# Optimization experiments

Hardware: AMD Instinct MI355X
Metric: run time of the kernel (lower is better)

The kernel has to match this reference:

```python
import jax, jax.numpy as jnp
import numpy as np

B, N, DIN, DOUT, H = 4, 2048, 512, 512, 8
HD = DOUT // H


def setup_inputs() -> dict:
    key = jax.random.key(0)
    ks = jax.random.split(key, 8)
    x = jax.random.normal(ks[0], (B, N, DIN), dtype=jnp.float32)
    mask = jax.random.randint(ks[1], (B, 1, N, N), 0, 2, dtype=jnp.int32)
    s = 1.0 / np.sqrt(DIN)
    Wq = jax.random.uniform(ks[2], (DOUT, DIN), jnp.float32, -s, s)
    Wk = jax.random.uniform(ks[3], (DOUT, DIN), jnp.float32, -s, s)
    Wv = jax.random.uniform(ks[4], (DOUT, DIN), jnp.float32, -s, s)
    bq = jax.random.uniform(ks[5], (DOUT,), jnp.float32, -s, s)
    bk = jax.random.uniform(ks[6], (DOUT,), jnp.float32, -s, s)
    bv = jax.random.uniform(ks[7], (DOUT,), jnp.float32, -s, s)
    return {"x": x, "Wq": Wq, "bq": bq, "Wk": Wk, "bk": bk, "Wv": Wv, "bv": bv, "mask": mask}


def reference(x, Wq, bq, Wk, bk, Wv, bv, mask):
    b, n, _ = x.shape
    # torch Linear: y = x @ W.T + b ; split heads -> [b, h, n, hd]
    def proj(W, bias):
        y = jnp.einsum('bnd,od->bno', x, W) + bias
        return y.reshape(b, n, H, HD).transpose(0, 2, 1, 3)
    Q, K, V = proj(Wq, bq), proj(Wk, bk), proj(Wv, bv)
    scores = jnp.einsum('bhnd,bhmd->bhnm', Q, K) / np.sqrt(HD).astype(np.float32)
    scores = jnp.where(mask == 0, jnp.float32(-1e9), scores)
    attn = jax.nn.softmax(scores, axis=-1)
    ctx = jnp.einsum('bhnm,bhmd->bhnd', attn, V)
    ctx = ctx.transpose(0, 2, 1, 3).reshape(b, n, DOUT)
    return jax.nn.elu(ctx)
```

## Files before the change

kernel.cpp:

```cpp
#include <hip/hip_runtime.h>
#include <math.h>
#include <stdint.h>

#define CB 4
#define CN 2048
#define CDIN 512
#define CDOUT 512
#define CH 8
#define CHD 64
#define CM (CB * CN)
#define CBH (CB * CH)
#define NKT (CN / 64)

typedef _Float16 f16x8 __attribute__((ext_vector_type(8)));
typedef _Float16 f16x4 __attribute__((ext_vector_type(4)));
typedef float    f32x4 __attribute__((ext_vector_type(4)));

#define QSCALE 0.1803368801111204f

#define PB_X  2048
#define PB_WQ 2176
#define PB_WK 2304
#define PB_WV 2432
#define PB_MB 3456

__global__ __launch_bounds__(256) void prep_kernel(
    const float* __restrict__ x,  _Float16* __restrict__ xh,
    const float* __restrict__ Wq, _Float16* __restrict__ wqh,
    const float* __restrict__ Wk, _Float16* __restrict__ wkh,
    const float* __restrict__ Wv, _Float16* __restrict__ wvh,
    const int* __restrict__ mask, unsigned long long* __restrict__ mbits)
{
    const int bx = blockIdx.x;
    if (bx >= PB_WV) {
        const int idx = (bx - PB_WV) * 256 + threadIdx.x;
        const int* src = mask + (size_t)idx * 64;
        unsigned long long m = 0;
        #pragma unroll
        for (int c = 0; c < 16; ++c) {
            int4 v = *(const int4*)&src[c * 4];
            unsigned long long bits = (v.x ? 1ull : 0ull) | (v.y ? 2ull : 0ull) |
                                      (v.z ? 4ull : 0ull) | (v.w ? 8ull : 0ull);
            m |= bits << (c * 4);
        }
        mbits[idx] = m;
        return;
    }
    const float* s; _Float16* d; int i;
    if (bx < PB_X)       { s = x;  d = xh;  i = bx * 2048 + threadIdx.x * 8; }
    else if (bx < PB_WQ) { s = Wq; d = wqh; i = (bx - PB_X)  * 2048 + threadIdx.x * 8; }
    else if (bx < PB_WK) { s = Wk; d = wkh; i = (bx - PB_WQ) * 2048 + threadIdx.x * 8; }
    else                 { s = Wv; d = wvh; i = (bx - PB_WK) * 2048 + threadIdx.x * 8; }
    float4 a = *(const float4*)&s[i];
    float4 b = *(const float4*)&s[i + 4];
    f16x8 h = {(_Float16)a.x, (_Float16)a.y, (_Float16)a.z, (_Float16)a.w,
               (_Float16)b.x, (_Float16)b.y, (_Float16)b.z, (_Float16)b.w};
    *(f16x8*)&d[i] = h;
}

__global__ __launch_bounds__(256) void proj_kernel(
    const _Float16* __restrict__ xh,
    const _Float16* __restrict__ Wqh, const float* __restrict__ bq,
    const _Float16* __restrict__ Wkh, const float* __restrict__ bk,
    const _Float16* __restrict__ Wvh, const float* __restrict__ bv,
    _Float16* __restrict__ Qf, _Float16* __restrict__ Kf, _Float16* __restrict__ Vt)
{
    const int z = blockIdx.z;
    const _Float16* W; const float* bias;
    if (z == 0)      { W = Wqh; bias = bq; }
    else if (z == 1) { W = Wkh; bias = bk; }
    else             { W = Wvh; bias = bv; }

    __shared__ _Float16 SM[2 * 128 * 72];

    const int tid  = threadIdx.x;
    const int m0   = blockIdx.x * 128;
    const int o0   = blockIdx.y * 128;
    const int lane = tid & 63, w = tid >> 6;
    const int il   = lane & 15, quad = lane >> 4;
    const int srow = tid >> 3, kc = (tid & 7) * 8;

    f32x4 acc[2][8] = {};
    f16x8 xr[4], wr[4];

    #pragma unroll
    for (int i = 0; i < 4; ++i) {
        xr[i] = *(const f16x8*)&xh[(size_t)(m0 + srow + i * 32) * CDIN + kc];
        wr[i] = *(const f16x8*)&W[(size_t)(o0 + srow + i * 32) * CDIN + kc];
    }

    for (int k0 = 0; k0 < CDIN; k0 += 64) {
        #pragma unroll
        for (int i = 0; i < 4; ++i) {
            *(f16x8*)&SM[(srow + i * 32) * 72 + kc] = xr[i];
            *(f16x8*)&SM[9216 + (srow + i * 32) * 72 + kc] = wr[i];
        }
        __syncthreads();

        if (k0 + 64 < CDIN) {
            #pragma unroll
            for (int i = 0; i < 4; ++i) {
                xr[i] = *(const f16x8*)&xh[(size_t)(m0 + srow + i * 32) * CDIN + k0 + 64 + kc];
                wr[i] = *(const f16x8*)&W[(size_t)(o0 + srow + i * 32) * CDIN + k0 + 64 + kc];
            }
        }

        #pragma unroll
        for (int dh = 0; dh < 2; ++dh) {
            f16x8 X0 = *(const f16x8*)&SM[(w * 32 + il) * 72 + dh * 32 + quad * 8];
            f16x8 X1 = *(const f16x8*)&SM[(w * 32 + 16 + il) * 72 + dh * 32 + quad * 8];
            if (z < 2) {
                #pragma unroll
                for (int s = 0; s < 8; ++s) {
                    f16x8 Wv_ = *(const f16x8*)&SM[9216 + (s * 16 + il) * 72 + dh * 32 + quad * 8];
                    acc[0][s] = __builtin_amdgcn_mfma_f32_16x16x32_f16(Wv_, X0, acc[0][s], 0, 0, 0);
                    acc[1][s] = __builtin_amdgcn_mfma_f32_16x16x32_f16(Wv_, X1, acc[1][s], 0, 0, 0);
                }
            } else {
                #pragma unroll
                for (int s = 0; s < 8; ++s) {
                    f16x8 Wv_ = *(const f16x8*)&SM[9216 + (s * 16 + il) * 72 + dh * 32 + quad * 8];
                    acc[0][s] = __builtin_amdgcn_mfma_f32_16x16x32_f16(X0, Wv_, acc[0][s], 0, 0, 0);
                    acc[1][s] = __builtin_amdgcn_mfma_f32_16x16x32_f16(X1, Wv_, acc[1][s], 0, 0, 0);
                }
            }
        }
        __syncthreads();
    }

    const int b  = m0 / CN;
    const int nb = m0 & (CN - 1);
    if (z < 2) {
        const float sc = (z == 0) ? QSCALE : 1.0f;
        #pragma unroll
        for (int s = 0; s < 8; ++s) {
            #pragma unroll
            for (int mi = 0; mi < 2; ++mi) {
                f16x4 pv;
                #pragma unroll
                for (int r = 0; r < 4; ++r)
                    pv[r] = (_Float16)((acc[mi][s][r] + bias[o0 + s * 16 + quad * 4 + r]) * sc);
                *(f16x4*)&SM[(w * 32 + mi * 16 + il) * 140 + s * 16 + quad * 4] = pv;
            }
        }
    } else {
        #pragma unroll
        for (int s = 0; s < 8; ++s) {
            const float bval = bias[o0 + s * 16 + il];
            #pragma unroll
            for (int mi = 0; mi < 2; ++mi) {
                f16x4 pv = {(_Float16)(acc[mi][s][0] + bval),
                            (_Float16)(acc[mi][s][1] + bval),
                            (_Float16)(acc[mi][s][2] + bval),
                            (_Float16)(acc[mi][s][3] + bval)};
                *(f16x4*)&SM[(s * 16 + il) * 140 + w * 32 + mi * 16 + quad * 4] = pv;
            }
        }
    }
    __syncthreads();

    const int uu   = tid & 127;
    const int hseg = tid >> 7;
    const int bh   = b * CH + (o0 >> 6) + hseg;
    if (z < 2) {
        _Float16* dst = ((z == 0) ? Qf : Kf) + ((size_t)bh * CN + nb) * CHD;
        #pragma unroll
        for (int k = 0; k < 8; ++k) {
            int n = k * 16 + (uu >> 3);
            int d = (uu & 7) * 8;
            *(f16x8*)&dst[(size_t)n * CHD + d] =
                *(const f16x8*)&SM[n * 140 + hseg * 64 + d];
        }
    } else {
        _Float16* dst = Vt + (size_t)bh * CHD * CN + nb;
        #pragma unroll
        for (int k = 0; k < 8; ++k) {
            int d = k * 8 + (uu >> 4);
            int n = (uu & 15) * 8;
            *(f16x8*)&dst[(size_t)d * CN + n] =
                *(const f16x8*)&SM[(hseg * 64 + d) * 140 + n];
        }
    }
}

__global__ __launch_bounds__(256) void attn_kernel(
    const _Float16* __restrict__ Qf, const _Float16* __restrict__ Kf,
    const _Float16* __restrict__ Vt, const unsigned long long* __restrict__ mbits,
    float* __restrict__ out)
{
    __shared__ _Float16 Ks[2][64][72];
    __shared__ _Float16 Vs[2][64][72];
    __shared__ _Float16 Ps[4][32][72];

    const int tid  = threadIdx.x;
    const int q0   = blockIdx.x * 128;
    const int bh   = blockIdx.y;
    const int b    = bh >> 3, h = bh & 7;
    const int lane = tid & 63, w = tid >> 6;
    const int il   = lane & 15, quad = lane >> 4;
    const int srow = tid >> 2, sc0 = (tid & 3) * 16;

    const _Float16* Qb = Qf + (size_t)bh * CN * CHD;
    const _Float16* Kb = Kf + (size_t)bh * CN * CHD;
    const _Float16* Vb = Vt + (size_t)bh * CHD * CN;

    const int qg0 = q0 + w * 32 + il;
    const int qg1 = qg0 + 16;
    const unsigned long long* mrow0 = mbits + ((size_t)b * CN + qg0) * NKT;
    const unsigned long long* mrow1 = mbits + ((size_t)b * CN + qg1) * NKT;

    f16x8 Qa0 = *(const f16x8*)&Qb[(size_t)qg0 * CHD + quad * 8];
    f16x8 Qa1 = *(const f16x8*)&Qb[(size_t)qg0 * CHD + 32 + quad * 8];
    f16x8 Qa2 = *(const f16x8*)&Qb[(size_t)qg1 * CHD + quad * 8];
    f16x8 Qa3 = *(const f16x8*)&Qb[(size_t)qg1 * CHD + 32 + quad * 8];

    const f16x8 ones = {1.f16, 1.f16, 1.f16, 1.f16, 1.f16, 1.f16, 1.f16, 1.f16};

    f32x4 oacc0[4] = {}, oacc1[4] = {};
    f32x4 lacc0 = {}, lacc1 = {};

    uint4 kA, kB, vA, vB; unsigned long long mn0, mn1;
    {
        const _Float16* kp = &Kb[(size_t)srow * CHD + sc0];
        const _Float16* vp = &Vb[(size_t)srow * CN + sc0];
        kA = *(const uint4*)kp; kB = *(const uint4*)(kp + 8);
        vA = *(const uint4*)vp; vB = *(const uint4*)(vp + 8);
        mn0 = mrow0[0]; mn1 = mrow1[0];
    }
    *(uint4*)&Ks[0][srow][sc0] = kA; *(uint4*)&Ks[0][srow][sc0 + 8] = kB;
    *(uint4*)&Vs[0][srow][sc0] = vA; *(uint4*)&Vs[0][srow][sc0 + 8] = vB;
    __syncthreads();

    for (int kt = 0; kt < NKT; ++kt) {
        const int cur = kt & 1;
        const unsigned long long mc0 = mn0, mc1 = mn1;

        if (kt < NKT - 1) {
            const _Float16* kp = &Kb[(size_t)((kt + 1) * 64 + srow) * CHD + sc0];
            const _Float16* vp = &Vb[(size_t)srow * CN + (kt + 1) * 64 + sc0];
            kA = *(const uint4*)kp; kB = *(const uint4*)(kp + 8);
            vA = *(const uint4*)vp; vB = *(const uint4*)(vp + 8);
            mn0 = mrow0[kt + 1]; mn1 = mrow1[kt + 1];
        }

        f32x4 st0[4] = {}, st1[4] = {};
        #pragma unroll
        for (int s = 0; s < 4; ++s) {
            f16x8 A0 = *(const f16x8*)&Ks[cur][s * 16 + il][quad * 8];
            f16x8 A1 = *(const f16x8*)&Ks[cur][s * 16 + il][32 + quad * 8];
            st0[s] = __builtin_amdgcn_mfma_f32_16x16x32_f16(A0, Qa0, st0[s], 0, 0, 0);
            st0[s] = __builtin_amdgcn_mfma_f32_16x16x32_f16(A1, Qa1, st0[s], 0, 0, 0);
            st1[s] = __builtin_amdgcn_mfma_f32_16x16x32_f16(A0, Qa2, st1[s], 0, 0, 0);
            st1[s] = __builtin_amdgcn_mfma_f32_16x16x32_f16(A1, Qa3, st1[s], 0, 0, 0);
        }

        const uint32_t m0lo = (uint32_t)mc0, m0hi = (uint32_t)(mc0 >> 32);
        const uint32_t m1lo = (uint32_t)mc1, m1hi = (uint32_t)(mc1 >> 32);
        #pragma unroll
        for (int s = 0; s < 4; ++s) {
            const uint32_t mm0 = (s < 2) ? m0lo : m0hi;
            const uint32_t mm1 = (s < 2) ? m1lo : m1hi;
            const int base = (s & 1) * 16 + quad * 4;
            f16x4 p0, p1;
            #pragma unroll
            for (int r = 0; r < 4; ++r) {
                float s0v = ((mm0 >> (base + r)) & 1u) ? st0[s][r] : -1e9f;
                float s1v = ((mm1 >> (base + r)) & 1u) ? st1[s][r] : -1e9f;
                p0[r] = (_Float16)__builtin_amdgcn_exp2f(s0v);
                p1[r] = (_Float16)__builtin_amdgcn_exp2f(s1v);
            }
            *(f16x4*)&Ps[w][il][s * 16 + quad * 4]      = p0;
            *(f16x4*)&Ps[w][16 + il][s * 16 + quad * 4] = p1;
        }

        f16x8 Pa00 = *(const f16x8*)&Ps[w][il][quad * 8];
        f16x8 Pa01 = *(const f16x8*)&Ps[w][il][32 + quad * 8];
        f16x8 Pa10 = *(const f16x8*)&Ps[w][16 + il][quad * 8];
        f16x8 Pa11 = *(const f16x8*)&Ps[w][16 + il][32 + quad * 8];
        #pragma unroll
        for (int s = 0; s < 4; ++s) {
            f16x8 B0 = *(const f16x8*)&Vs[cur][s * 16 + il][quad * 8];
            f16x8 B1 = *(const f16x8*)&Vs[cur][s * 16 + il][32 + quad * 8];
            oacc0[s] = __builtin_amdgcn_mfma_f32_16x16x32_f16(Pa00, B0, oacc0[s], 0, 0, 0);
            oacc0[s] = __builtin_amdgcn_mfma_f32_16x16x32_f16(Pa01, B1, oacc0[s], 0, 0, 0);
            oacc1[s] = __builtin_amdgcn_mfma_f32_16x16x32_f16(Pa10, B0, oacc1[s], 0, 0, 0);
            oacc1[s] = __builtin_amdgcn_mfma_f32_16x16x32_f16(Pa11, B1, oacc1[s], 0, 0, 0);
        }
        lacc0 = __builtin_amdgcn_mfma_f32_16x16x32_f16(Pa00, ones, lacc0, 0, 0, 0);
        lacc0 = __builtin_amdgcn_mfma_f32_16x16x32_f16(Pa01, ones, lacc0, 0, 0, 0);
        lacc1 = __builtin_amdgcn_mfma_f32_16x16x32_f16(Pa10, ones, lacc1, 0, 0, 0);
        lacc1 = __builtin_amdgcn_mfma_f32_16x16x32_f16(Pa11, ones, lacc1, 0, 0, 0);

        if (kt < NKT - 1) {
            *(uint4*)&Ks[cur ^ 1][srow][sc0] = kA;
            *(uint4*)&Ks[cur ^ 1][srow][sc0 + 8] = kB;
            *(uint4*)&Vs[cur ^ 1][srow][sc0] = vA;
            *(uint4*)&Vs[cur ^ 1][srow][sc0 + 8] = vB;
            __syncthreads();
        }
    }

    #pragma unroll
    for (int s = 0; s < 4; ++s) {
        const int d = h * CHD + s * 16 + il;
        #pragma unroll
        for (int r = 0; r < 4; ++r) {
            int n0 = q0 + w * 32 + quad * 4 + r;
            float c0 = oacc0[s][r] / lacc0[r];
            out[((size_t)b * CN + n0) * CDOUT + d] = c0 > 0.f ? c0 : expm1f(c0);
            int n1 = n0 + 16;
            float c1 = oacc1[s][r] / lacc1[r];
            out[((size_t)b * CN + n1) * CDOUT + d] = c1 > 0.f ? c1 : expm1f(c1);
        }
    }
}

extern "C" void kernel_launch(void* const* d_in, const int* in_sizes, int n_in,
                              void* d_out, int out_size, void* d_ws, size_t ws_size,
                              hipStream_t stream) {
    const float* x    = (const float*)d_in[0];
    const float* Wq   = (const float*)d_in[1];
    const float* bq   = (const float*)d_in[2];
    const float* Wk   = (const float*)d_in[3];
    const float* bk   = (const float*)d_in[4];
    const float* Wv   = (const float*)d_in[5];
    const float* bv   = (const float*)d_in[6];
    const int*   mask = (const int*)d_in[7];
    float* out = (float*)d_out;

    const size_t nx = (size_t)CM * CDIN;
    const size_t nw = (size_t)CDOUT * CDIN;
    const size_t nt = (size_t)CBH * CN * CHD;
    _Float16* xh  = (_Float16*)d_ws;
    _Float16* wqh = xh + nx;
    _Float16* wkh = wqh + nw;
    _Float16* wvh = wkh + nw;
    _Float16* Qf  = wvh + nw;
    _Float16* Kf  = Qf + nt;
    _Float16* Vt  = Kf + nt;
    unsigned long long* mbits = (unsigned long long*)(Vt + nt);

    prep_kernel<<<dim3(PB_MB), 256, 0, stream>>>(
        x, xh, Wq, wqh, Wk, wkh, Wv, wvh, mask, mbits);
    proj_kernel<<<dim3(CM / 128, CDOUT / 128, 3), 256, 0, stream>>>(
        xh, wqh, bq, wkh, bk, wvh, bv, Qf, Kf, Vt);
    attn_kernel<<<dim3(CN / 128, CBH), 256, 0, stream>>>(
        Qf, Kf, Vt, mbits, out);
}
```

Measured before the change: 230.0 us.

## Use 8 waves of 16 query rows in attention; pack mask via ballot

The attention kernel now launches 512 threads per block, with each wave handling 16 query rows instead of 32. This halves per-wave accumulator registers and spreads the K/V tile loads across more threads, aiming for higher occupancy and better latency hiding. The mask packing in the prep kernel now reads the mask coalesced across a wave and uses __ballot to form each 64-bit word, replacing per-thread strided int4 reads. The trade-off is less reuse of each K/V shared-memory fragment per wave and more barrier participants.

```diff
diff --git a/kernel.cpp b/kernel.cpp
--- a/kernel.cpp
+++ b/kernel.cpp
@@ -33,17 +33,17 @@
 {
     const int bx = blockIdx.x;
     if (bx >= PB_WV) {
-        const int idx = (bx - PB_WV) * 256 + threadIdx.x;
-        const int* src = mask + (size_t)idx * 64;
-        unsigned long long m = 0;
-        #pragma unroll
-        for (int c = 0; c < 16; ++c) {
-            int4 v = *(const int4*)&src[c * 4];
-            unsigned long long bits = (v.x ? 1ull : 0ull) | (v.y ? 2ull : 0ull) |
-                                      (v.z ? 4ull : 0ull) | (v.w ? 8ull : 0ull);
-            m |= bits << (c * 4);
-        }
-        mbits[idx] = m;
+        const int lane = threadIdx.x & 63;
+        const int wv   = threadIdx.x >> 6;
+        const int wbase = (bx - PB_WV) * 256 + wv * 64;
+        unsigned long long myword = 0;
+        #pragma unroll 8
+        for (int it = 0; it < 64; ++it) {
+            int v = mask[(size_t)(wbase + it) * 64 + lane];
+            unsigned long long bal = __ballot(v != 0);
+            if (lane == it) myword = bal;
+        }
+        mbits[wbase + lane] = myword;
         return;
     }
     const float* s; _Float16* d; int i;
@@ -183,14 +183,14 @@
     }
 }
 
-__global__ __launch_bounds__(256) void attn_kernel(
+__global__ __launch_bounds__(512, 4) void attn_kernel(
     const _Float16* __restrict__ Qf, const _Float16* __restrict__ Kf,
     const _Float16* __restrict__ Vt, const unsigned long long* __restrict__ mbits,
     float* __restrict__ out)
 {
     __shared__ _Float16 Ks[2][64][72];
     __shared__ _Float16 Vs[2][64][72];
-    __shared__ _Float16 Ps[4][32][72];
+    __shared__ _Float16 Ps[8][16][72];
 
     const int tid  = threadIdx.x;
     const int q0   = blockIdx.x * 128;
@@ -198,104 +198,79 @@
     const int b    = bh >> 3, h = bh & 7;
     const int lane = tid & 63, w = tid >> 6;
     const int il   = lane & 15, quad = lane >> 4;
-    const int srow = tid >> 2, sc0 = (tid & 3) * 16;
+    const int srow = tid >> 3, sc0 = (tid & 7) * 8;
 
     const _Float16* Qb = Qf + (size_t)bh * CN * CHD;
     const _Float16* Kb = Kf + (size_t)bh * CN * CHD;
     const _Float16* Vb = Vt + (size_t)bh * CHD * CN;
 
-    const int qg0 = q0 + w * 32 + il;
-    const int qg1 = qg0 + 16;
-    const unsigned long long* mrow0 = mbits + ((size_t)b * CN + qg0) * NKT;
-    const unsigned long long* mrow1 = mbits + ((size_t)b * CN + qg1) * NKT;
-
-    f16x8 Qa0 = *(const f16x8*)&Qb[(size_t)qg0 * CHD + quad * 8];
-    f16x8 Qa1 = *(const f16x8*)&Qb[(size_t)qg0 * CHD + 32 + quad * 8];
-    f16x8 Qa2 = *(const f16x8*)&Qb[(size_t)qg1 * CHD + quad * 8];
-    f16x8 Qa3 = *(const f16x8*)&Qb[(size_t)qg1 * CHD + 32 + quad * 8];
+    const int qg = q0 + w * 16 + il;
+    const unsigned long long* mrow = mbits + ((size_t)b * CN + qg) * NKT;
+
+    f16x8 Qa0 = *(const f16x8*)&Qb[(size_t)qg * CHD + quad * 8];
+    f16x8 Qa1 = *(const f16x8*)&Qb[(size_t)qg * CHD + 32 + quad * 8];
 
     const f16x8 ones = {1.f16, 1.f16, 1.f16, 1.f16, 1.f16, 1.f16, 1.f16, 1.f16};
 
-    f32x4 oacc0[4] = {}, oacc1[4] = {};
-    f32x4 lacc0 = {}, lacc1 = {};
-
-    uint4 kA, kB, vA, vB; unsigned long long mn0, mn1;
-    {
-        const _Float16* kp = &Kb[(size_t)srow * CHD + sc0];
-        const _Float16* vp = &Vb[(size_t)srow * CN + sc0];
-        kA = *(const uint4*)kp; kB = *(const uint4*)(kp + 8);
-        vA = *(const uint4*)vp; vB = *(const uint4*)(vp + 8);
-        mn0 = mrow0[0]; mn1 = mrow1[0];
-    }
-    *(uint4*)&Ks[0][srow][sc0] = kA; *(uint4*)&Ks[0][srow][sc0 + 8] = kB;
-    *(uint4*)&Vs[0][srow][sc0] = vA; *(uint4*)&Vs[0][srow][sc0 + 8] = vB;
+    f32x4 oacc[4] = {};
+    f32x4 lacc = {};
+
+    uint4 kA, vA; unsigned long long mn;
+    kA = *(const uint4*)&Kb[(size_t)srow * CHD + sc0];
+    vA = *(const uint4*)&Vb[(size_t)srow * CN + sc0];
+    mn = mrow[0];
+    *(uint4*)&Ks[0][srow][sc0] = kA;
+    *(uint4*)&Vs[0][srow][sc0] = vA;
     __syncthreads();
 
     for (int kt = 0; kt < NKT; ++kt) {
         const int cur = kt & 1;
-        const unsigned long long mc0 = mn0, mc1 = mn1;
+        const unsigned long long mcur = mn;
 
         if (kt < NKT - 1) {
-            const _Float16* kp = &Kb[(size_t)((kt + 1) * 64 + srow) * CHD + sc0];
-            const _Float16* vp = &Vb[(size_t)srow * CN + (kt + 1) * 64 + sc0];
-            kA = *(const uint4*)kp; kB = *(const uint4*)(kp + 8);
-            vA = *(const uint4*)vp; vB = *(const uint4*)(vp + 8);
-            mn0 = mrow0[kt + 1]; mn1 = mrow1[kt + 1];
-        }
-
-        f32x4 st0[4] = {}, st1[4] = {};
+            kA = *(const uint4*)&Kb[(size_t)((kt + 1) * 64 + srow) * CHD + sc0];
+            vA = *(const uint4*)&Vb[(size_t)srow * CN + (kt + 1) * 64 + sc0];
+            mn = mrow[kt + 1];
+        }
+
+        f32x4 st[4] = {};
         #pragma unroll
         for (int s = 0; s < 4; ++s) {
             f16x8 A0 = *(const f16x8*)&Ks[cur][s * 16 + il][quad * 8];
             f16x8 A1 = *(const f16x8*)&Ks[cur][s * 16 + il][32 + quad * 8];
-            st0[s] = __builtin_amdgcn_mfma_f32_16x16x32_f16(A0, Qa0, st0[s], 0, 0, 0);
-            st0[s] = __builtin_amdgcn_mfma_f32_16x16x32_f16(A1, Qa1, st0[s], 0, 0, 0);
-            st1[s] = __builtin_amdgcn_mfma_f32_16x16x32_f16(A0, Qa2, st1[s], 0, 0, 0);
-            st1[s] = __builtin_amdgcn_mfma_f32_16x16x32_f16(A1, Qa3, st1[s], 0, 0, 0);
-        }
-
-        const uint32_t m0lo = (uint32_t)mc0, m0hi = (uint32_t)(mc0 >> 32);
-        const uint32_t m1lo = (uint32_t)mc1, m1hi = (uint32_t)(mc1 >> 32);
+            st[s] = __builtin_amdgcn_mfma_f32_16x16x32_f16(A0, Qa0, st[s], 0, 0, 0);
+            st[s] = __builtin_amdgcn_mfma_f32_16x16x32_f16(A1, Qa1, st[s], 0, 0, 0);
+        }
+
+        const uint32_t mlo = (uint32_t)mcur, mhi = (uint32_t)(mcur >> 32);
         #pragma unroll
         for (int s = 0; s < 4; ++s) {
-            const uint32_t mm0 = (s < 2) ? m0lo : m0hi;
-            const uint32_t mm1 = (s < 2) ? m1lo : m1hi;
+            const uint32_t mm = (s < 2) ? mlo : mhi;
             const int base = (s & 1) * 16 + quad * 4;
-            f16x4 p0, p1;
+            f16x4 pv;
             #pragma unroll
             for (int r = 0; r < 4; ++r) {
-                float s0v = ((mm0 >> (base + r)) & 1u) ? st0[s][r] : -1e9f;
-                float s1v = ((mm1 >> (base + r)) & 1u) ? st1[s][r] : -1e9f;
-                p0[r] = (_Float16)__builtin_amdgcn_exp2f(s0v);
-                p1[r] = (_Float16)__builtin_amdgcn_exp2f(s1v);
-            }
-            *(f16x4*)&Ps[w][il][s * 16 + quad * 4]      = p0;
-            *(f16x4*)&Ps[w][16 + il][s * 16 + quad * 4] = p1;
-        }
-
-        f16x8 Pa00 = *(const f16x8*)&Ps[w][il][quad * 8];
-        f16x8 Pa01 = *(const f16x8*)&Ps[w][il][32 + quad * 8];
-        f16x8 Pa10 = *(const f16x8*)&Ps[w][16 + il][quad * 8];
-        f16x8 Pa11 = *(const f16x8*)&Ps[w][16 + il][32 + quad * 8];
+                float sv = ((mm >> (base + r)) & 1u) ? st[s][r] : -1e9f;
+                pv[r] = (_Float16)__builtin_amdgcn_exp2f(sv);
+            }
+            *(f16x4*)&Ps[w][il][s * 16 + quad * 4] = pv;
+        }
+
+        f16x8 Pa0 = *(const f16x8*)&Ps[w][il][quad * 8];
+        f16x8 Pa1 = *(const f16x8*)&Ps[w][il][32 + quad * 8];
         #pragma unroll
         for (int s = 0; s < 4; ++s) {
             f16x8 B0 = *(const f16x8*)&Vs[cur][s * 16 + il][quad * 8];
             f16x8 B1 = *(const f16x8*)&Vs[cur][s * 16 + il][32 + quad * 8];
-            oacc0[s] = __builtin_amdgcn_mfma_f32_16x16x32_f16(Pa00, B0, oacc0[s], 0, 0, 0);
-            oacc0[s] = __builtin_amdgcn_mfma_f32_16x16x32_f16(Pa01, B1, oacc0[s], 0, 0, 0);
-            oacc1[s] = __builtin_amdgcn_mfma_f32_16x16x32_f16(Pa10, B0, oacc1[s], 0, 0, 0);
-            oacc1[s] = __builtin_amdgcn_mfma_f32_16x16x32_f16(Pa11, B1, oacc1[s], 0, 0, 0);
-        }
-        lacc0 = __builtin_amdgcn_mfma_f32_16x16x32_f16(Pa00, ones, lacc0, 0, 0, 0);
-        lacc0 = __builtin_amdgcn_mfma_f32_16x16x32_f16(Pa01, ones, lacc0, 0, 0, 0);
-        lacc1 = __builtin_amdgcn_mfma_f32_16x16x32_f16(Pa10, ones, lacc1, 0, 0, 0);
-        lacc1 = __builtin_amdgcn_mfma_f32_16x16x32_f16(Pa11, ones, lacc1, 0, 0, 0);
+            oacc[s] = __builtin_amdgcn_mfma_f32_16x16x32_f16(Pa0, B0, oacc[s], 0, 0, 0);
+            oacc[s] = __builtin_amdgcn_mfma_f32_16x16x32_f16(Pa1, B1, oacc[s], 0, 0, 0);
+        }
+        lacc = __builtin_amdgcn_mfma_f32_16x16x32_f16(Pa0, ones, lacc, 0, 0, 0);
+        lacc = __builtin_amdgcn_mfma_f32_16x16x32_f16(Pa1, ones, lacc, 0, 0, 0);
 
         if (kt < NKT - 1) {
             *(uint4*)&Ks[cur ^ 1][srow][sc0] = kA;
-            *(uint4*)&Ks[cur ^ 1][srow][sc0 + 8] = kB;
             *(uint4*)&Vs[cur ^ 1][srow][sc0] = vA;
-            *(uint4*)&Vs[cur ^ 1][srow][sc0 + 8] = vB;
             __syncthreads();
         }
     }
@@ -305,12 +280,9 @@
         const int d = h * CHD + s * 16 + il;
         #pragma unroll
         for (int r = 0; r < 4; ++r) {
-            int n0 = q0 + w * 32 + quad * 4 + r;
-            float c0 = oacc0[s][r] / lacc0[r];
-            out[((size_t)b * CN + n0) * CDOUT + d] = c0 > 0.f ? c0 : expm1f(c0);
-            int n1 = n0 + 16;
-            float c1 = oacc1[s][r] / lacc1[r];
-            out[((size_t)b * CN + n1) * CDOUT + d] = c1 > 0.f ? c1 : expm1f(c1);
+            int n = q0 + w * 16 + quad * 4 + r;
+            float c = oacc[s][r] / lacc[r];
+            out[((size_t)b * CN + n) * CDOUT + d] = c > 0.f ? c : expm1f(c);
         }
     }
 }
@@ -344,6 +316,6 @@
         x, xh, Wq, wqh, Wk, wkh, Wv, wvh, mask, mbits);
     proj_kernel<<<dim3(CM / 128, CDOUT / 128, 3), 256, 0, stream>>>(
         xh, wqh, bq, wkh, bk, wvh, bv, Qf, Kf, Vt);
-    attn_kernel<<<dim3(CN / 128, CBH), 256, 0, stream>>>(
+    attn_kernel<<<dim3(CN / 128, CBH), 512, 0, stream>>>(
         Qf, Kf, Vt, mbits, out);
 }
```

Result: faster. 211.6 us (-8.0%).
